# Kernel optimization log

Measured on AMD Instinct MI355X. Metric: run time of the kernel, lower is better.

## Reference

```python
import math
import jax, jax.numpy as jnp
import numpy as np

D_MODEL = 1024
L_MAX = 4096
BATCH = 2
FILTER_ORDER = 64
EMB_DIM = 3


def _make_z(L, emb_dim=EMB_DIM):
    # PositionalEmbedding: [time, real bands, imag bands] -> [1, L, emb_dim]
    t = jnp.linspace(0.0, 1.0, L)[None, :, None]
    bands = (emb_dim - 1) // 2
    t_res = jnp.linspace(0.0, L - 1.0, L)[None, :, None]
    w = 2.0 * math.pi * t_res / L
    f = jnp.linspace(1e-4, float(bands - 1), bands)[None, None]
    ph = f * w  # z = exp(-1j*ph) -> real=cos(ph), imag=-sin(ph)
    return jnp.concatenate([t, jnp.cos(ph), -jnp.sin(ph)], axis=-1).astype(jnp.float32)


def setup_inputs() -> dict:
    key = jax.random.key(0)
    ks = jax.random.split(key, 16)
    d = D_MODEL
    iw = 3 * d  # inner_width = d_model * (order + 1), order=2

    def rn(k, shape, scale):
        return (jax.random.normal(k, shape) * scale).astype(jnp.float32)

    return {
        'u': rn(ks[0], (BATCH, L_MAX, d), 1.0),
        'w_in': rn(ks[1], (iw, d), d ** -0.5),
        'b_in': rn(ks[2], (iw,), 0.01),
        'sf_w': rn(ks[3], (iw, 1, 3), 3 ** -0.5),
        'sf_b': rn(ks[4], (iw,), 0.01),
        'z': _make_z(L_MAX),
        'w0': rn(ks[5], (FILTER_ORDER, EMB_DIM), EMB_DIM ** -0.5),
        'b0': rn(ks[6], (FILTER_ORDER,), 0.01),
        'freq': jnp.ones((1, FILTER_ORDER), dtype=jnp.float32),  # Sin(w=1)
        'w1': rn(ks[7], (FILTER_ORDER, FILTER_ORDER), FILTER_ORDER ** -0.5),
        'b1': rn(ks[8], (FILTER_ORDER,), 0.01),
        'w2': rn(ks[9], (FILTER_ORDER, FILTER_ORDER), FILTER_ORDER ** -0.5),
        'b2': rn(ks[10], (FILTER_ORDER,), 0.01),
        'wf': rn(ks[11], (d, FILTER_ORDER), FILTER_ORDER ** -0.5),
        'D': rn(ks[12], (d,), 1.0),
        'w_out': rn(ks[13], (d, d), d ** -0.5),
        'b_out': rn(ks[14], (d,), 0.01),
    }


def _dwconv(x, w, b):
    # depthwise Conv1d(kernel=3, padding=2, groups=C); x: [B, C, L] -> [B, C, L+2]
    y = jax.lax.conv_general_dilated(
        x, w, window_strides=(1,), padding=[(2, 2)],
        feature_group_count=x.shape[1],
        dimension_numbers=('NCH', 'OIH', 'NCH'))
    return y + b[None, :, None]


def _fftconv(v, k, D):
    # circular conv via zero-padded FFT; torch's k_f/fft_size with norm='forward'
    # irfft cancels to the standard (norm='backward') inverse.
    L = v.shape[-1]
    n = 2 * L
    y = jnp.fft.irfft(jnp.fft.rfft(v, n=n) * jnp.fft.rfft(k, n=n), n=n)[..., :L]
    return y + v * D[:, None]


def reference(u, w_in, b_in, sf_w, sf_b, z, w0, b0, freq, w1, b1, w2, b2, wf, D, w_out, b_out):
    b, l, d = u.shape
    L = min(l, L_MAX)

    # input projection + short depthwise filter
    up = jnp.einsum('bld,ed->ble', u, w_in) + b_in  # [b, l, 3d]
    up = up.transpose(0, 2, 1)                       # [b, 3d, l]
    uc = _dwconv(up, sf_w, sf_b)[..., :L]            # [b, 3d, L]
    x0, x1, v = jnp.split(uc, 3, axis=1)             # each [b, d, L]

    # implicit filter MLP with shared Sin activation
    h = jnp.sin(freq * (z @ w0.T + b0))              # [1, L, 64]
    h = jnp.sin(freq * (h @ w1.T + b1))
    h = jnp.sin(freq * (h @ w2.T + b2))
    h = h @ wf.T                                     # [1, L, d]

    # exponential modulation (buffers: t, deltas)
    t = jnp.linspace(0.0, 1.0, L)[None, :, None]
    max_decay = math.log(0.01) / 0.3
    min_decay = math.log(0.01) / 1.5
    deltas = jnp.linspace(min_decay, max_decay, d)[None, None]
    h = h * jnp.exp(-t * jnp.abs(deltas))            # [1, L, d]
    k = h[0].T                                       # [d, L]

    # hyena recurrence (order=2 -> one gated fft conv)
    v = _fftconv(v * x1, k, D)
    y = (v * x0).transpose(0, 2, 1)                  # [b, L, d]
    return jnp.einsum('bld,ed->ble', y, w_out) + b_out
```

## Files before the change

kernel.cpp:

```cpp
#include <hip/hip_runtime.h>
#include <math.h>

#define DM   1024
#define LL   4096
#define NB   2
#define E3   3072
#define FPI  3.14159265358979323846f

typedef __bf16 bf16x8 __attribute__((ext_vector_type(8)));
typedef float  f32x4  __attribute__((ext_vector_type(4)));
typedef _Float16 f16x2 __attribute__((ext_vector_type(2)));

__device__ __forceinline__ unsigned short f2bf(float x) {
    unsigned u = __float_as_uint(x);
    u += 0x7fffu + ((u >> 16) & 1u);
    return (unsigned short)(u >> 16);
}
__device__ __forceinline__ float bf2f(ushort s) {
    return __uint_as_float(((unsigned)s) << 16);
}
__device__ __forceinline__ void gload16(void* lds, const void* g) {
    typedef const __attribute__((address_space(1))) unsigned int* gp_t;
    typedef __attribute__((address_space(3))) unsigned int* lp_t;
    __builtin_amdgcn_global_load_lds((gp_t)g, (lp_t)lds, 16, 0, 0);
}

__global__ __launch_bounds__(256) void k_cvt3(
    const float* __restrict__ a, ushort* __restrict__ oa, int n4a,
    const float* __restrict__ b, ushort* __restrict__ ob, int n4b,
    const float* __restrict__ c, ushort* __restrict__ oc, int n4c)
{
    int idx = blockIdx.x * 256 + threadIdx.x;
    int stride = gridDim.x * 256;
    int tot = n4a + n4b + n4c;
    for (int i = idx; i < tot; i += stride) {
        const float4* src; ushort* dst; int k;
        if (i < n4a)            { src = (const float4*)a; dst = oa; k = i; }
        else if (i < n4a + n4b) { src = (const float4*)b; dst = ob; k = i - n4a; }
        else                    { src = (const float4*)c; dst = oc; k = i - n4a - n4b; }
        float4 v = src[k];
        ushort4 o;
        o.x = f2bf(v.x); o.y = f2bf(v.y); o.z = f2bf(v.z); o.w = f2bf(v.w);
        *reinterpret_cast<ushort4*>(dst + 4 * k) = o;
    }
}

__global__ __launch_bounds__(512, 1) void k_gemm128n(
    const ushort* __restrict__ A, const ushort* __restrict__ B,
    const float* __restrict__ bias, ushort* __restrict__ C,
    int Ntiles, int ldc)
{
    __shared__ __align__(16) char ldsm[98304];
    const int tid  = threadIdx.x;
    const int lane = tid & 63;
    const int w    = tid >> 6;
    const int wr   = w >> 2, wc = w & 3;

    const int cpx = gridDim.x >> 3;
    int swz = (blockIdx.x & 7) * cpx + (blockIdx.x >> 3);
    const int m0 = (swz / Ntiles) << 7;
    const int n0 = (swz % Ntiles) << 8;

    const int r0 = tid >> 2;
    const int swzc = ((tid & 3) ^ ((r0 >> 1) & 3)) << 4;
    const char* Asrc = (const char*)A + ((size_t)(m0 + r0) << 11) + swzc;
    const char* Bsrc = (const char*)B + ((size_t)(n0 + r0) << 11) + swzc;
    char* Ld = ldsm + tid * 16;

    const int lm = lane & 15, lk = lane >> 4;
    const int rA = wr * 64 + lm;
    const int rB = wc * 64 + lm;
    const int aBase = rA * 64 + ((lk ^ ((rA >> 1) & 3)) << 4);
    const int bBase = 16384 + rB * 64 + ((lk ^ ((rB >> 1) & 3)) << 4);

#define STG_A(ks, nb, t1) \
    gload16(Ld + (nb) + (ks)*8192, Asrc + (t1)*128 + (ks)*64)
#define STG_B(ks, nb, t1) do { \
    gload16(Ld + (nb) + 16384 + (ks)*16384,        Bsrc + (t1)*128 + (ks)*64); \
    gload16(Ld + (nb) + 16384 + (ks)*16384 + 8192, Bsrc + (t1)*128 + (ks)*64 + 262144); } while(0)
#define LDA(buf, ks, m) (*(const bf16x8*)(ldsm + (buf) + (ks)*8192 + aBase + (m)*1024))
#define LDB(buf, ks, n) (*(const bf16x8*)(ldsm + (buf) + (ks)*16384 + bBase + (n)*1024))
#define VMCNT3() asm volatile("s_waitcnt vmcnt(3)" ::: "memory")
#define VMCNT0() asm volatile("s_waitcnt vmcnt(0)" ::: "memory")
#define BAR() __builtin_amdgcn_s_barrier()

    f32x4 acc[4][4];
#pragma unroll
    for (int i = 0; i < 4; ++i)
#pragma unroll
        for (int j = 0; j < 4; ++j)
#pragma unroll
            for (int r = 0; r < 4; ++r) acc[i][j][r] = 0.f;

    STG_A(0, 0, 0); STG_B(0, 0, 0); STG_A(1, 0, 0); STG_B(1, 0, 0);
    VMCNT3();
    BAR();

    bf16x8 af[2], bq[4];
#pragma unroll 1
    for (int t = 0; t < 15; ++t) {
        const int buf = (t & 1) * 49152;
        const int nb  = 49152 - buf;
        const int t1  = t + 1;
#pragma unroll
        for (int n = 0; n < 4; ++n) bq[n] = LDB(buf, 0, n);
        af[0] = LDA(buf, 0, 0); af[1] = LDA(buf, 0, 1);
        STG_A(0, nb, t1);
        BAR();
        __builtin_amdgcn_s_setprio(1);
#pragma unroll
        for (int m = 0; m < 2; ++m)
#pragma unroll
            for (int n = 0; n < 4; ++n)
                acc[m][n] = __builtin_amdgcn_mfma_f32_16x16x32_bf16(af[m], bq[n], acc[m][n], 0, 0, 0);
        __builtin_amdgcn_s_setprio(0);
        BAR();
        af[0] = LDA(buf, 0, 2); af[1] = LDA(buf, 0, 3);
        STG_B(0, nb, t1);
        VMCNT3();
        BAR();
        __builtin_amdgcn_s_setprio(1);
#pragma unroll
        for (int m = 0; m < 2; ++m)
#pragma unroll
            for (int n = 0; n < 4; ++n)
                acc[2 + m][n] = __builtin_amdgcn_mfma_f32_16x16x32_bf16(af[m], bq[n], acc[2 + m][n], 0, 0, 0);
        __builtin_amdgcn_s_setprio(0);
        BAR();
#pragma unroll
        for (int n = 0; n < 4; ++n) bq[n] = LDB(buf, 1, n);
        af[0] = LDA(buf, 1, 0); af[1] = LDA(buf, 1, 1);
        STG_A(1, nb, t1);
        BAR();
        __builtin_amdgcn_s_setprio(1);
#pragma unroll
        for (int m = 0; m < 2; ++m)
#pragma unroll
            for (int n = 0; n < 4; ++n)
                acc[m][n] = __builtin_amdgcn_mfma_f32_16x16x32_bf16(af[m], bq[n], acc[m][n], 0, 0, 0);
        __builtin_amdgcn_s_setprio(0);
        BAR();
        af[0] = LDA(buf, 1, 2); af[1] = LDA(buf, 1, 3);
        STG_B(1, nb, t1);
        VMCNT3();
        BAR();
        __builtin_amdgcn_s_setprio(1);
#pragma unroll
        for (int m = 0; m < 2; ++m)
#pragma unroll
            for (int n = 0; n < 4; ++n)
                acc[2 + m][n] = __builtin_amdgcn_mfma_f32_16x16x32_bf16(af[m], bq[n], acc[2 + m][n], 0, 0, 0);
        __builtin_amdgcn_s_setprio(0);
        BAR();
    }
    {
        const int buf = 49152;
#pragma unroll
        for (int n = 0; n < 4; ++n) bq[n] = LDB(buf, 0, n);
        af[0] = LDA(buf, 0, 0); af[1] = LDA(buf, 0, 1);
#pragma unroll
        for (int m = 0; m < 2; ++m)
#pragma unroll
            for (int n = 0; n < 4; ++n)
                acc[m][n] = __builtin_amdgcn_mfma_f32_16x16x32_bf16(af[m], bq[n], acc[m][n], 0, 0, 0);
        af[0] = LDA(buf, 0, 2); af[1] = LDA(buf, 0, 3);
#pragma unroll
        for (int m = 0; m < 2; ++m)
#pragma unroll
            for (int n = 0; n < 4; ++n)
                acc[2 + m][n] = __builtin_amdgcn_mfma_f32_16x16x32_bf16(af[m], bq[n], acc[2 + m][n], 0, 0, 0);
        VMCNT0();
        BAR();
#pragma unroll
        for (int n = 0; n < 4; ++n) bq[n] = LDB(buf, 1, n);
        af[0] = LDA(buf, 1, 0); af[1] = LDA(buf, 1, 1);
#pragma unroll
        for (int m = 0; m < 2; ++m)
#pragma unroll
            for (int n = 0; n < 4; ++n)
                acc[m][n] = __builtin_amdgcn_mfma_f32_16x16x32_bf16(af[m], bq[n], acc[m][n], 0, 0, 0);
        af[0] = LDA(buf, 1, 2); af[1] = LDA(buf, 1, 3);
#pragma unroll
        for (int m = 0; m < 2; ++m)
#pragma unroll
            for (int n = 0; n < 4; ++n)
                acc[2 + m][n] = __builtin_amdgcn_mfma_f32_16x16x32_bf16(af[m], bq[n], acc[2 + m][n], 0, 0, 0);
    }
    const int er = lk << 2, ec = lm;
#pragma unroll
    for (int m = 0; m < 4; ++m) {
        int row = m0 + wr * 64 + m * 16 + er;
#pragma unroll
        for (int n = 0; n < 4; ++n) {
            int col = n0 + wc * 64 + n * 16 + ec;
            ushort* cp = C + (size_t)row * ldc + col;
#pragma unroll
            for (int r = 0; r < 4; ++r)
                cp[(size_t)r * ldc] = f2bf(acc[m][n][r] + bias[row + r]);
        }
    }
#undef STG_A
#undef STG_B
#undef LDA
#undef LDB
#undef VMCNT3
#undef VMCNT0
#undef BAR
}

__global__ __launch_bounds__(256) void k_gemm_bf16(
    const ushort* __restrict__ A, const ushort* __restrict__ B,
    const float* __restrict__ bias, float* __restrict__ C, int ldc)
{
    __shared__ ushort As[128 * 32];
    __shared__ ushort Bs[128 * 32];
    const int tid  = threadIdx.x;
    const int lane = tid & 63;
    const int w    = tid >> 6;
    const int wm   = (w >> 1) << 6, wn = (w & 1) << 6;
    const int m0   = blockIdx.y << 7, n0 = blockIdx.x << 7;

    f32x4 acc[4][4];
#pragma unroll
    for (int i = 0; i < 4; ++i)
#pragma unroll
        for (int j = 0; j < 4; ++j)
#pragma unroll
            for (int r = 0; r < 4; ++r) acc[i][j][r] = 0.f;

    const char* Ab = (const char*)A + ((size_t)(m0 + (tid >> 2)) << 11) + ((tid & 3) << 4);
    const char* Bb = (const char*)B + ((size_t)(n0 + (tid >> 2)) << 11) + ((tid & 3) << 4);
    char* AsD = (char*)As + tid * 16;
    char* BsD = (char*)Bs + tid * 16;
    const char* ap = (const char*)As + ((wm + (lane & 15)) << 6) + ((lane >> 4) << 4);
    const char* bp = (const char*)Bs + ((wn + (lane & 15)) << 6) + ((lane >> 4) << 4);

    for (int k0 = 0; k0 < 1024; k0 += 32) {
        __syncthreads();
        gload16(AsD,        Ab + k0 * 2);
        gload16(AsD + 4096, Ab + 131072 + k0 * 2);
        gload16(BsD,        Bb + k0 * 2);
        gload16(BsD + 4096, Bb + 131072 + k0 * 2);
        __syncthreads();
        bf16x8 af[4], bfr[4];
#pragma unroll
        for (int i = 0; i < 4; ++i) {
            af[i]  = *(const bf16x8*)(ap + (i << 10));
            bfr[i] = *(const bf16x8*)(bp + (i << 10));
        }
#pragma unroll
        for (int i = 0; i < 4; ++i)
#pragma unroll
            for (int j = 0; j < 4; ++j)
                acc[i][j] = __builtin_amdgcn_mfma_f32_16x16x32_bf16(
                    af[i], bfr[j], acc[i][j], 0, 0, 0);
    }
    const int er = (lane >> 4) << 2;
    const int ec = lane & 15;
#pragma unroll
    for (int i = 0; i < 4; ++i) {
        int row = m0 + wm + (i << 4) + er;
#pragma unroll
        for (int j = 0; j < 4; ++j) {
            int col = n0 + wn + (j << 4) + ec;
            float bz = bias[col];
            float* cp = C + (size_t)row * ldc + col;
#pragma unroll
            for (int r = 0; r < 4; ++r)
                cp[(size_t)r * ldc] = acc[i][j][r] + bz;
        }
    }
}

__global__ __launch_bounds__(256) void k_filt_mlp(
    const float* __restrict__ z, const float* __restrict__ w0,
    const float* __restrict__ b0, const float* __restrict__ fr,
    const float* __restrict__ w1, const float* __restrict__ b1,
    const float* __restrict__ w2, const float* __restrict__ b2,
    float* __restrict__ H3)
{
    __shared__ float w1t[64 * 65];
    __shared__ float w2t[64 * 65];
    __shared__ float hb[4][64];
    const int tid = threadIdx.x;
    for (int idx = tid; idx < 4096; idx += 256) {
        int j = idx >> 6, m = idx & 63;
        w1t[m*65 + j] = w1[idx];
        w2t[m*65 + j] = w2[idx];
    }
    __syncthreads();
    const int tl = tid >> 6, j = tid & 63;
    const float frj = fr[j];
    const float b0j = b0[j], b1j = b1[j], b2j = b2[j];
    const float w00 = w0[j*3+0], w01 = w0[j*3+1], w02 = w0[j*3+2];
    const int t0 = blockIdx.x * 16;
    for (int r = 0; r < 4; ++r) {
        int t = t0 + r*4 + tl;
        float z0 = z[t*3+0], z1 = z[t*3+1], z2 = z[t*3+2];
        float h = sinf(frj * (b0j + z0*w00 + z1*w01 + z2*w02));
        hb[tl][j] = h;
        __syncthreads();
        float s = b1j;
#pragma unroll
        for (int m = 0; m < 64; ++m) s = fmaf(hb[tl][m], w1t[m*65 + j], s);
        __syncthreads();
        h = sinf(frj * s);
        hb[tl][j] = h;
        __syncthreads();
        s = b2j;
#pragma unroll
        for (int m = 0; m < 64; ++m) s = fmaf(hb[tl][m], w2t[m*65 + j], s);
        h = sinf(frj * s);
        H3[(size_t)t * 64 + j] = h;
        __syncthreads();
    }
}

__global__ __launch_bounds__(256) void k_filt_k(
    const float* __restrict__ H3, const float* __restrict__ wf,
    float* __restrict__ kf)
{
    __shared__ float Hs[64][65];
    __shared__ float Ws[64][65];
    const int tid = threadIdx.x;
    const int t0 = blockIdx.x * 64, d0 = blockIdx.y * 64;
    for (int idx = tid; idx < 4096; idx += 256) {
        int r = idx >> 6, cc = idx & 63;
        Hs[r][cc] = H3[(size_t)(t0 + r) * 64 + cc];
        Ws[r][cc] = wf[(size_t)(d0 + r) * 64 + cc];
    }
    __syncthreads();
    const int tx = tid & 15, ty = tid >> 4;
    float acc[4][4];
#pragma unroll
    for (int i = 0; i < 4; ++i)
#pragma unroll
        for (int jj = 0; jj < 4; ++jj) acc[i][jj] = 0.f;
#pragma unroll
    for (int j = 0; j < 64; ++j) {
        float wv[4], hv[4];
#pragma unroll
        for (int i = 0; i < 4; ++i) wv[i] = Ws[4*ty + i][j];
#pragma unroll
        for (int i = 0; i < 4; ++i) hv[i] = Hs[4*tx + i][j];
#pragma unroll
        for (int i = 0; i < 4; ++i)
#pragma unroll
            for (int jj = 0; jj < 4; ++jj) acc[i][jj] = fmaf(wv[i], hv[jj], acc[i][jj]);
    }
    const float mind = -3.0701134573253944f;
    const float maxd = -15.350567286626972f;
#pragma unroll
    for (int i = 0; i < 4; ++i) {
        int d = d0 + 4*ty + i;
        float delta = fabsf(mind + (maxd - mind) * ((float)d / 1023.f));
#pragma unroll
        for (int jj = 0; jj < 4; ++jj) {
            int t = t0 + 4*tx + jj;
            float tn = (float)t / 4095.f;
            kf[(size_t)d * LL + t] = acc[i][jj] * expf(-tn * delta);
        }
    }
}

__device__ __forceinline__ int pidx(int p) { return p + (p >> 4); }

__device__ __forceinline__ float2 cmul(float2 a, float2 b) {
    return make_float2(a.x*b.x - a.y*b.y, a.x*b.y + a.y*b.x);
}

__device__ void fft_lds_fwd4(float2* buf, int tid) {
    int lh = 10;
#pragma unroll
    for (int h = 2048; h >= 32; h >>= 2, lh -= 2) {
        const int hh = h >> 1;
        const float rinv = -FPI / (float)h;
        __syncthreads();
#pragma unroll
        for (int r = 0; r < 4; ++r) {
            int bf = (r << 9) + tid;
            int q  = bf & (hh - 1);
            int g  = bf >> lh;
            int j  = (g << (lh + 2)) + q;
            float2 a = buf[pidx(j)];
            float2 b = buf[pidx(j + hh)];
            float2 c = buf[pidx(j + h)];
            float2 d = buf[pidx(j + h + hh)];
            float2 t0 = make_float2(a.x + c.x, a.y + c.y);
            float2 t1 = make_float2(a.x - c.x, a.y - c.y);
            float2 t2 = make_float2(b.x + d.x, b.y + d.y);
            float2 t3 = make_float2(b.y - d.y, d.x - b.x);
            float sn, cs;
            __sincosf(rinv * (float)q, &sn, &cs);
            float c2 = cs*cs - sn*sn, s2 = 2.f*cs*sn;
            float c3 = cs*c2 - sn*s2, s3 = cs*s2 + sn*c2;
            buf[pidx(j)] = make_float2(t0.x + t2.x, t0.y + t2.y);
            float2 e1 = make_float2(t0.x - t2.x, t0.y - t2.y);
            buf[pidx(j + hh)] = make_float2(e1.x*c2 - e1.y*s2, e1.x*s2 + e1.y*c2);
            float2 e2 = make_float2(t1.x + t3.x, t1.y + t3.y);
            buf[pidx(j + h)] = make_float2(e2.x*cs - e2.y*sn, e2.x*sn + e2.y*cs);
            float2 e3 = make_float2(t1.x - t3.x, t1.y - t3.y);
            buf[pidx(j + h + hh)] = make_float2(e3.x*c3 - e3.y*s3, e3.x*s3 + e3.y*c3);
        }
    }
    __syncthreads();
}

__device__ void fft_lds_inv4(float2* buf, int tid) {
    int lh = 4;
#pragma unroll
    for (int h = 32; h <= 2048; h <<= 2, lh += 2) {
        const int hh = h >> 1;
        const float rpos = FPI / (float)h;
        __syncthreads();
#pragma unroll
        for (int r = 0; r < 4; ++r) {
            int bf = (r << 9) + tid;
            int q  = bf & (hh - 1);
            int g  = bf >> lh;
            int j  = (g << (lh + 2)) + q;
            float2 o0 = buf[pidx(j)];
            float2 o1 = buf[pidx(j + hh)];
            float2 o2 = buf[pidx(j + h)];
            float2 o3 = buf[pidx(j + h + hh)];
            float sn, cs;
            __sincosf(rpos * (float)q, &sn, &cs);
            float c2 = cs*cs - sn*sn, s2 = 2.f*cs*sn;
            float c3 = cs*c2 - sn*s2, s3 = cs*s2 + sn*c2;
            float2 p1 = make_float2(o1.x*c2 - o1.y*s2, o1.x*s2 + o1.y*c2);
            float2 p2 = make_float2(o2.x*cs - o2.y*sn, o2.x*sn + o2.y*cs);
            float2 p3 = make_float2(o3.x*c3 - o3.y*s3, o3.x*s3 + o3.y*c3);
            float2 u0 = make_float2(o0.x + p1.x, o0.y + p1.y);
            float2 u1 = make_float2(o0.x - p1.x, o0.y - p1.y);
            float2 u2 = make_float2(p2.x + p3.x, p2.y + p3.y);
            float2 u3 = make_float2(p2.x - p3.x, p2.y - p3.y);
            float2 ib = make_float2(-u3.y, u3.x);
            buf[pidx(j)]          = make_float2(u0.x + u2.x, u0.y + u2.y);
            buf[pidx(j + hh)]     = make_float2(u1.x + ib.x, u1.y + ib.y);
            buf[pidx(j + h)]      = make_float2(u0.x - u2.x, u0.y - u2.y);
            buf[pidx(j + h + hh)] = make_float2(u1.x - ib.x, u1.y - ib.y);
        }
    }
    __syncthreads();
}

__device__ __forceinline__ void fft_reg_fwd(float2* c) {
    const float W16r[8] = {1.f, 0.92387953f, 0.70710678f, 0.38268343f,
                           0.f, -0.38268343f, -0.70710678f, -0.92387953f};
    const float W16i[8] = {0.f, -0.38268343f, -0.70710678f, -0.92387953f,
                           -1.f, -0.92387953f, -0.70710678f, -0.38268343f};
#pragma unroll
    for (int k = 0; k < 8; ++k) {
        float2 a = c[k], b = c[k+8];
        float2 d = make_float2(a.x - b.x, a.y - b.y);
        c[k]   = make_float2(a.x + b.x, a.y + b.y);
        c[k+8] = cmul(d, make_float2(W16r[k], W16i[k]));
    }
    const float W8r[4] = {1.f, 0.70710678f, 0.f, -0.70710678f};
    const float W8i[4] = {0.f, -0.70710678f, -1.f, -0.70710678f};
#pragma unroll
    for (int blk = 0; blk < 16; blk += 8)
#pragma unroll
        for (int k = 0; k < 4; ++k) {
            float2 a = c[blk+k], b = c[blk+k+4];
            float2 d = make_float2(a.x - b.x, a.y - b.y);
            c[blk+k]   = make_float2(a.x + b.x, a.y + b.y);
            c[blk+k+4] = cmul(d, make_float2(W8r[k], W8i[k]));
        }
#pragma unroll
    for (int blk = 0; blk < 16; blk += 4) {
        {   float2 a = c[blk], b = c[blk+2];
            c[blk]   = make_float2(a.x + b.x, a.y + b.y);
            c[blk+2] = make_float2(a.x - b.x, a.y - b.y); }
        {   float2 a = c[blk+1], b = c[blk+3];
            float2 d = make_float2(a.x - b.x, a.y - b.y);
            c[blk+1] = make_float2(a.x + b.x, a.y + b.y);
            c[blk+3] = make_float2(d.y, -d.x); }
    }
#pragma unroll
    for (int blk = 0; blk < 16; blk += 2) {
        float2 a = c[blk], b = c[blk+1];
        c[blk]   = make_float2(a.x + b.x, a.y + b.y);
        c[blk+1] = make_float2(a.x - b.x, a.y - b.y);
    }
}

__device__ __forceinline__ void fft_reg_inv(float2* c) {
#pragma unroll
    for (int blk = 0; blk < 16; blk += 2) {
        float2 a = c[blk], b = c[blk+1];
        c[blk]   = make_float2(a.x + b.x, a.y + b.y);
        c[blk+1] = make_float2(a.x - b.x, a.y - b.y);
    }
#pragma unroll
    for (int blk = 0; blk < 16; blk += 4) {
        {   float2 a = c[blk], b = c[blk+2];
            c[blk]   = make_float2(a.x + b.x, a.y + b.y);
            c[blk+2] = make_float2(a.x - b.x, a.y - b.y); }
        {   float2 a = c[blk+1], b = c[blk+3];
            float2 bt = make_float2(-c[blk+3].y, c[blk+3].x);
            c[blk+1] = make_float2(a.x + bt.x, a.y + bt.y);
            c[blk+3] = make_float2(a.x - bt.x, a.y - bt.y); }
    }
    const float W8r[4] = {1.f, 0.70710678f, 0.f, -0.70710678f};
    const float W8i[4] = {0.f, 0.70710678f, 1.f, 0.70710678f};
#pragma unroll
    for (int blk = 0; blk < 16; blk += 8)
#pragma unroll
        for (int k = 0; k < 4; ++k) {
            float2 a = c[blk+k], b = c[blk+k+4];
            float2 bt = cmul(b, make_float2(W8r[k], W8i[k]));
            c[blk+k]   = make_float2(a.x + bt.x, a.y + bt.y);
            c[blk+k+4] = make_float2(a.x - bt.x, a.y - bt.y);
        }
    const float W16r[8] = {1.f, 0.92387953f, 0.70710678f, 0.38268343f,
                           0.f, -0.38268343f, -0.70710678f, -0.92387953f};
    const float W16i[8] = {0.f, 0.38268343f, 0.70710678f, 0.92387953f,
                           1.f, 0.92387953f, 0.70710678f, 0.38268343f};
#pragma unroll
    for (int k = 0; k < 8; ++k) {
        float2 a = c[k], b = c[k+8];
        float2 bt = cmul(b, make_float2(W16r[k], W16i[k]));
        c[k]   = make_float2(a.x + bt.x, a.y + bt.y);
        c[k+8] = make_float2(a.x - bt.x, a.y - bt.y);
    }
}

__global__ __launch_bounds__(512) void k_kfft(
    const float* __restrict__ kf, f16x2* __restrict__ Kf)
{
    __shared__ float2 buf[8704];
    const int d = blockIdx.x, tid = threadIdx.x;
    const float* krow = kf + (size_t)d * LL;
    const float rinv0 = -FPI / 4096.f;
    for (int i = tid; i < 1024; i += 512) {
        float4 k4 = reinterpret_cast<const float4*>(krow)[i];
        int p = 4 * i;
        float kv[4] = {k4.x, k4.y, k4.z, k4.w};
#pragma unroll
        for (int q = 0; q < 4; ++q) {
            float sn, cs;
            __sincosf(rinv0 * (float)(p + q), &sn, &cs);
            buf[pidx(p + q)]        = make_float2(kv[q], 0.f);
            buf[pidx(p + q + 4096)] = make_float2(kv[q] * cs, kv[q] * sn);
        }
    }
    fft_lds_fwd4(buf, tid);
    float2 c[16];
    const int p0 = tid * 16;
#pragma unroll
    for (int j = 0; j < 16; ++j) c[j] = buf[pidx(p0 + j)];
    fft_reg_fwd(c);
    f16x2* outp = Kf + (size_t)d * 8192 + p0;
#pragma unroll
    for (int j = 0; j < 16; ++j) {
        f16x2 o;
        o[0] = (_Float16)(c[j].x * (1.f/8192.f));
        o[1] = (_Float16)(c[j].y * (1.f/8192.f));
        outp[j] = o;
    }
}

__device__ __forceinline__ void conv4(const ushort* __restrict__ row, int p,
    float w0, float w1, float w2, float bias, float* out)
{
    float xm2, xm1;
    if (p >= 2) {
        unsigned prev = *reinterpret_cast<const unsigned*>(row + p - 2);
        xm2 = bf2f((ushort)(prev & 0xffffu));
        xm1 = bf2f((ushort)(prev >> 16));
    } else { xm2 = 0.f; xm1 = 0.f; }
    uint2 cur = *reinterpret_cast<const uint2*>(row + p);
    float x0 = bf2f((ushort)(cur.x & 0xffffu));
    float x1 = bf2f((ushort)(cur.x >> 16));
    float x2 = bf2f((ushort)(cur.y & 0xffffu));
    float x3 = bf2f((ushort)(cur.y >> 16));
    out[0] = fmaf(w2, x0, fmaf(w1, xm1, fmaf(w0, xm2, bias)));
    out[1] = fmaf(w2, x1, fmaf(w1, x0,  fmaf(w0, xm1, bias)));
    out[2] = fmaf(w2, x2, fmaf(w1, x1,  fmaf(w0, x0,  bias)));
    out[3] = fmaf(w2, x3, fmaf(w1, x2,  fmaf(w0, x1,  bias)));
}

__global__ __launch_bounds__(512) void k_fftconv(
    const ushort* __restrict__ up2, const f16x2* __restrict__ Kf,
    const float* __restrict__ sfw, const float* __restrict__ sfb,
    const float* __restrict__ Dp, ushort* __restrict__ yg)
{
    __shared__ float2 buf[8704];
    const int d = blockIdx.x, tid = threadIdx.x;
    const ushort* vrow0  = up2 + (size_t)(2048 + d) * 8192;
    const ushort* vrow1  = vrow0 + 4096;
    const ushort* x1row0 = up2 + (size_t)(1024 + d) * 8192;
    const ushort* x1row1 = x1row0 + 4096;
    const ushort* x0row0 = up2 + (size_t)d * 8192;
    const ushort* x0row1 = x0row0 + 4096;
    const float wv0 = sfw[(2048+d)*3+0], wv1 = sfw[(2048+d)*3+1],
                wv2 = sfw[(2048+d)*3+2], bv = sfb[2048+d];
    const float wx0 = sfw[(1024+d)*3+0], wx1 = sfw[(1024+d)*3+1],
                wx2 = sfw[(1024+d)*3+2], bx = sfb[1024+d];
    const float g0 = sfw[d*3+0], g1 = sfw[d*3+1], g2 = sfw[d*3+2], bg = sfb[d];
    const float rinv0 = -FPI / 4096.f;

    float vs0[8], vs1[8];
#pragma unroll
    for (int ii = 0; ii < 2; ++ii) {
        int p = 4 * tid + ii * 2048;
        float cv0[4], cv1[4], cx0[4], cx1[4];
        conv4(vrow0,  p, wv0, wv1, wv2, bv, cv0);
        conv4(vrow1,  p, wv0, wv1, wv2, bv, cv1);
        conv4(x1row0, p, wx0, wx1, wx2, bx, cx0);
        conv4(x1row1, p, wx0, wx1, wx2, bx, cx1);
#pragma unroll
        for (int q = 0; q < 4; ++q) {
            float z0 = cv0[q] * cx0[q];
            float z1 = cv1[q] * cx1[q];
            vs0[ii*4 + q] = z0;
            vs1[ii*4 + q] = z1;
            float sn, cs;
            __sincosf(rinv0 * (float)(p + q), &sn, &cs);
            float2 z = make_float2(z0, z1);
            buf[pidx(p + q)]        = z;
            buf[pidx(p + q + 4096)] = cmul(z, make_float2(cs, sn));
        }
    }
    fft_lds_fwd4(buf, tid);
    float2 c[16];
    const int p0 = tid * 16;
#pragma unroll
    for (int j = 0; j < 16; ++j) c[j] = buf[pidx(p0 + j)];
    fft_reg_fwd(c);
    const f16x2* kfr = Kf + (size_t)d * 8192 + p0;
#pragma unroll
    for (int j = 0; j < 16; ++j) {
        f16x2 kv = kfr[j];
        c[j] = cmul(c[j], make_float2((float)kv[0], (float)kv[1]));
    }
    fft_reg_inv(c);
#pragma unroll
    for (int j = 0; j < 16; ++j) buf[pidx(p0 + j)] = c[j];
    fft_lds_inv4(buf, tid);
    const float Dd = Dp[d];
    ushort* orow0 = yg + (size_t)d * LL;
    ushort* orow1 = yg + ((size_t)DM + d) * LL;
    const float rinv4 = FPI / 4096.f;
#pragma unroll
    for (int ii = 0; ii < 2; ++ii) {
        int p = 4 * tid + ii * 2048;
        float cg0[4], cg1[4];
        conv4(x0row0, p, g0, g1, g2, bg, cg0);
        conv4(x0row1, p, g0, g1, g2, bg, cg1);
        ushort s0[4], s1[4];
#pragma unroll
        for (int q = 0; q < 4; ++q) {
            float sn, cs;
            __sincosf(rinv4 * (float)(p + q), &sn, &cs);
            float2 a  = buf[pidx(p + q)];
            float2 bb = buf[pidx(p + q + 4096)];
            float2 bt = cmul(bb, make_float2(cs, sn));
            s0[q] = f2bf((a.x + bt.x + Dd * vs0[ii*4 + q]) * cg0[q]);
            s1[q] = f2bf((a.y + bt.y + Dd * vs1[ii*4 + q]) * cg1[q]);
        }
        *reinterpret_cast<ushort4*>(orow0 + p) = make_ushort4(s0[0], s0[1], s0[2], s0[3]);
        *reinterpret_cast<ushort4*>(orow1 + p) = make_ushort4(s1[0], s1[1], s1[2], s1[3]);
    }
}

__global__ __launch_bounds__(256) void k_tr(
    const ushort* __restrict__ yg, ushort* __restrict__ Ag)
{
    __shared__ ushort S[64][72];
    const int b  = blockIdx.z;
    const int d0 = blockIdx.y * 64;
    const int t0 = blockIdx.x * 64;
    const int tid = threadIdx.x;
#pragma unroll
    for (int p = 0; p < 2; ++p) {
        int idx = p * 256 + tid;
        int dr = idx >> 3, c8 = (idx & 7) << 3;
        uint4 v = *reinterpret_cast<const uint4*>(
            yg + ((size_t)b * DM + d0 + dr) * LL + t0 + c8);
        *reinterpret_cast<uint4*>(&S[dr][c8]) = v;
    }
    __syncthreads();
#pragma unroll
    for (int p = 0; p < 2; ++p) {
        int idx = p * 256 + tid;
        int tr = idx >> 3, dq = (idx & 7) << 3;
        ushort tmp[8] __attribute__((aligned(16)));
#pragma unroll
        for (int q = 0; q < 8; ++q) tmp[q] = S[dq + q][tr];
        *reinterpret_cast<uint4*>(Ag + ((size_t)b * LL + t0 + tr) * DM + d0 + dq) =
            *reinterpret_cast<uint4*>(tmp);
    }
}

extern "C" void kernel_launch(void* const* d_in, const int* in_sizes, int n_in,
                              void* d_out, int out_size, void* d_ws, size_t ws_size,
                              hipStream_t stream)
{
    if (n_in < 17) return;
    const float* u    = (const float*)d_in[0];
    const float* w_in = (const float*)d_in[1];
    const float* b_in = (const float*)d_in[2];
    const float* sf_w = (const float*)d_in[3];
    const float* sf_b = (const float*)d_in[4];
    const float* z    = (const float*)d_in[5];
    const float* w0   = (const float*)d_in[6];
    const float* b0   = (const float*)d_in[7];
    const float* freq = (const float*)d_in[8];
    const float* w1   = (const float*)d_in[9];
    const float* b1   = (const float*)d_in[10];
    const float* w2   = (const float*)d_in[11];
    const float* b2   = (const float*)d_in[12];
    const float* wf   = (const float*)d_in[13];
    const float* Dp   = (const float*)d_in[14];
    const float* wout = (const float*)d_in[15];
    const float* bout = (const float*)d_in[16];
    float* out = (float*)d_out;
    float* ws  = (float*)d_ws;

    ushort* up2   = (ushort*)ws;
    float*  kfbuf = ws + 16777216;
    ushort* yg    = (ushort*)(ws + 16777216);
    float*  H3    = ws + 20971520;
    ushort* Ag    = (ushort*)(ws + 20971520);
    ushort* ub    = (ushort*)(ws + 25165824);
    ushort* wb    = (ushort*)(ws + 33554432);
    f16x2*  Kf    = (f16x2*)(ws + 33554432);
    ushort* woutb = (ushort*)(ws + 41943040);
    const size_t NEED = (size_t)(41943040 + 524288) * 4;
    if (ws_size < NEED) return;

    hipLaunchKernelGGL(k_cvt3,     dim3(2048), dim3(256), 0, stream,
                       u, ub, 2097152, w_in, wb, 786432, wout, woutb, 262144);
    hipLaunchKernelGGL(k_gemm128n, dim3((E3/128) * (8192/256)), dim3(512), 0, stream,
                       wb, ub, b_in, up2, 8192/256, 8192);
    hipLaunchKernelGGL(k_filt_mlp, dim3(LL/16), dim3(256), 0, stream,
                       z, w0, b0, freq, w1, b1, w2, b2, H3);
    hipLaunchKernelGGL(k_filt_k,   dim3(LL/64, DM/64), dim3(256), 0, stream,
                       H3, wf, kfbuf);
    hipLaunchKernelGGL(k_kfft,     dim3(DM), dim3(512), 0, stream,
                       kfbuf, Kf);
    hipLaunchKernelGGL(k_fftconv,  dim3(DM), dim3(512), 0, stream,
                       up2, Kf, sf_w, sf_b, Dp, yg);
    hipLaunchKernelGGL(k_tr,       dim3(LL/64, DM/64, NB), dim3(256), 0, stream,
                       yg, Ag);
    hipLaunchKernelGGL(k_gemm_bf16, dim3(DM/128, 8192/128), dim3(256), 0, stream,
                       Ag, woutb, bout, out, DM);
}
```

Baseline: 223.8 us.

## Fuse filter FFT into fftconv kernel and remap GEMM tiles per XCD

The separate k_kfft kernel is removed. Each fftconv block now computes its own filter spectrum in LDS and keeps it in registers, which drops the fp16 spectrum write and read and one kernel launch. To limit register pressure, the saved v*x1 values are recomputed from up2 in the epilogue instead of being held across the FFTs. The input-projection GEMM's block-to-tile mapping is changed so each XCD owns a contiguous range of N tiles. The costs are more VGPR use from the 16 held complex values and extra reloads for the recompute.

Result: no change. 224.3 us (+0.2%).

```diff
diff --git a/kernel.cpp b/kernel.cpp
--- a/kernel.cpp
+++ b/kernel.cpp
@@ -9,7 +9,6 @@
 
 typedef __bf16 bf16x8 __attribute__((ext_vector_type(8)));
 typedef float  f32x4  __attribute__((ext_vector_type(4)));
-typedef _Float16 f16x2 __attribute__((ext_vector_type(2)));
 
 __device__ __forceinline__ unsigned short f2bf(float x) {
     unsigned u = __float_as_uint(x);
@@ -56,10 +55,11 @@
     const int w    = tid >> 6;
     const int wr   = w >> 2, wc = w & 3;
 
-    const int cpx = gridDim.x >> 3;
-    int swz = (blockIdx.x & 7) * cpx + (blockIdx.x >> 3);
-    const int m0 = (swz / Ntiles) << 7;
-    const int n0 = (swz % Ntiles) << 8;
+    const int nch = Ntiles >> 3;
+    const int xcd = blockIdx.x & 7;
+    const int loc = blockIdx.x >> 3;
+    const int n0 = ((xcd * nch) + (loc % nch)) << 8;
+    const int m0 = (loc / nch) << 7;
 
     const int r0 = tid >> 2;
     const int swzc = ((tid & 3) ^ ((r0 >> 1) & 3)) << 4;
@@ -526,41 +526,6 @@
     }
 }
 
-__global__ __launch_bounds__(512) void k_kfft(
-    const float* __restrict__ kf, f16x2* __restrict__ Kf)
-{
-    __shared__ float2 buf[8704];
-    const int d = blockIdx.x, tid = threadIdx.x;
-    const float* krow = kf + (size_t)d * LL;
-    const float rinv0 = -FPI / 4096.f;
-    for (int i = tid; i < 1024; i += 512) {
-        float4 k4 = reinterpret_cast<const float4*>(krow)[i];
-        int p = 4 * i;
-        float kv[4] = {k4.x, k4.y, k4.z, k4.w};
-#pragma unroll
-        for (int q = 0; q < 4; ++q) {
-            float sn, cs;
-            __sincosf(rinv0 * (float)(p + q), &sn, &cs);
-            buf[pidx(p + q)]        = make_float2(kv[q], 0.f);
-            buf[pidx(p + q + 4096)] = make_float2(kv[q] * cs, kv[q] * sn);
-        }
-    }
-    fft_lds_fwd4(buf, tid);
-    float2 c[16];
-    const int p0 = tid * 16;
-#pragma unroll
-    for (int j = 0; j < 16; ++j) c[j] = buf[pidx(p0 + j)];
-    fft_reg_fwd(c);
-    f16x2* outp = Kf + (size_t)d * 8192 + p0;
-#pragma unroll
-    for (int j = 0; j < 16; ++j) {
-        f16x2 o;
-        o[0] = (_Float16)(c[j].x * (1.f/8192.f));
-        o[1] = (_Float16)(c[j].y * (1.f/8192.f));
-        outp[j] = o;
-    }
-}
-
 __device__ __forceinline__ void conv4(const ushort* __restrict__ row, int p,
     float w0, float w1, float w2, float bias, float* out)
 {
@@ -582,12 +547,40 @@
 }
 
 __global__ __launch_bounds__(512) void k_fftconv(
-    const ushort* __restrict__ up2, const f16x2* __restrict__ Kf,
+    const float* __restrict__ kfrow_all, const ushort* __restrict__ up2,
     const float* __restrict__ sfw, const float* __restrict__ sfb,
     const float* __restrict__ Dp, ushort* __restrict__ yg)
 {
     __shared__ float2 buf[8704];
     const int d = blockIdx.x, tid = threadIdx.x;
+    const float rinv0 = -FPI / 4096.f;
+    const int p0 = tid * 16;
+
+    {
+        const float* krow = kfrow_all + (size_t)d * LL;
+#pragma unroll
+        for (int ii = 0; ii < 2; ++ii) {
+            int i = tid + ii * 512;
+            float4 k4 = reinterpret_cast<const float4*>(krow)[i];
+            int p = 4 * i;
+            float kv[4] = {k4.x * (1.f/8192.f), k4.y * (1.f/8192.f),
+                           k4.z * (1.f/8192.f), k4.w * (1.f/8192.f)};
+#pragma unroll
+            for (int q = 0; q < 4; ++q) {
+                float sn, cs;
+                __sincosf(rinv0 * (float)(p + q), &sn, &cs);
+                buf[pidx(p + q)]        = make_float2(kv[q], 0.f);
+                buf[pidx(p + q + 4096)] = make_float2(kv[q] * cs, kv[q] * sn);
+            }
+        }
+    }
+    fft_lds_fwd4(buf, tid);
+    float2 ks[16];
+#pragma unroll
+    for (int j = 0; j < 16; ++j) ks[j] = buf[pidx(p0 + j)];
+    fft_reg_fwd(ks);
+    __syncthreads();
+
     const ushort* vrow0  = up2 + (size_t)(2048 + d) * 8192;
     const ushort* vrow1  = vrow0 + 4096;
     const ushort* x1row0 = up2 + (size_t)(1024 + d) * 8192;
@@ -599,9 +592,7 @@
     const float wx0 = sfw[(1024+d)*3+0], wx1 = sfw[(1024+d)*3+1],
                 wx2 = sfw[(1024+d)*3+2], bx = sfb[1024+d];
     const float g0 = sfw[d*3+0], g1 = sfw[d*3+1], g2 = sfw[d*3+2], bg = sfb[d];
-    const float rinv0 = -FPI / 4096.f;
-
-    float vs0[8], vs1[8];
+
 #pragma unroll
     for (int ii = 0; ii < 2; ++ii) {
         int p = 4 * tid + ii * 2048;
@@ -614,8 +605,6 @@
         for (int q = 0; q < 4; ++q) {
             float z0 = cv0[q] * cx0[q];
             float z1 = cv1[q] * cx1[q];
-            vs0[ii*4 + q] = z0;
-            vs1[ii*4 + q] = z1;
             float sn, cs;
             __sincosf(rinv0 * (float)(p + q), &sn, &cs);
             float2 z = make_float2(z0, z1);
@@ -625,16 +614,11 @@
     }
     fft_lds_fwd4(buf, tid);
     float2 c[16];
-    const int p0 = tid * 16;
 #pragma unroll
     for (int j = 0; j < 16; ++j) c[j] = buf[pidx(p0 + j)];
     fft_reg_fwd(c);
-    const f16x2* kfr = Kf + (size_t)d * 8192 + p0;
-#pragma unroll
-    for (int j = 0; j < 16; ++j) {
-        f16x2 kv = kfr[j];
-        c[j] = cmul(c[j], make_float2((float)kv[0], (float)kv[1]));
-    }
+#pragma unroll
+    for (int j = 0; j < 16; ++j) c[j] = cmul(c[j], ks[j]);
     fft_reg_inv(c);
 #pragma unroll
     for (int j = 0; j < 16; ++j) buf[pidx(p0 + j)] = c[j];
@@ -646,9 +630,13 @@
 #pragma unroll
     for (int ii = 0; ii < 2; ++ii) {
         int p = 4 * tid + ii * 2048;
-        float cg0[4], cg1[4];
+        float cg0[4], cg1[4], cv0[4], cv1[4], cx0[4], cx1[4];
         conv4(x0row0, p, g0, g1, g2, bg, cg0);
         conv4(x0row1, p, g0, g1, g2, bg, cg1);
+        conv4(vrow0,  p, wv0, wv1, wv2, bv, cv0);
+        conv4(vrow1,  p, wv0, wv1, wv2, bv, cv1);
+        conv4(x1row0, p, wx0, wx1, wx2, bx, cx0);
+        conv4(x1row1, p, wx0, wx1, wx2, bx, cx1);
         ushort s0[4], s1[4];
 #pragma unroll
         for (int q = 0; q < 4; ++q) {
@@ -657,8 +645,8 @@
             float2 a  = buf[pidx(p + q)];
             float2 bb = buf[pidx(p + q + 4096)];
             float2 bt = cmul(bb, make_float2(cs, sn));
-            s0[q] = f2bf((a.x + bt.x + Dd * vs0[ii*4 + q]) * cg0[q]);
-            s1[q] = f2bf((a.y + bt.y + Dd * vs1[ii*4 + q]) * cg1[q]);
+            s0[q] = f2bf((a.x + bt.x + Dd * cv0[q] * cx0[q]) * cg0[q]);
+            s1[q] = f2bf((a.y + bt.y + Dd * cv1[q] * cx1[q]) * cg1[q]);
         }
         *reinterpret_cast<ushort4*>(orow0 + p) = make_ushort4(s0[0], s0[1], s0[2], s0[3]);
         *reinterpret_cast<ushort4*>(orow1 + p) = make_ushort4(s1[0], s1[1], s1[2], s1[3]);
@@ -721,12 +709,11 @@
 
     ushort* up2   = (ushort*)ws;
     float*  kfbuf = ws + 16777216;
-    ushort* yg    = (ushort*)(ws + 16777216);
     float*  H3    = ws + 20971520;
     ushort* Ag    = (ushort*)(ws + 20971520);
     ushort* ub    = (ushort*)(ws + 25165824);
     ushort* wb    = (ushort*)(ws + 33554432);
-    f16x2*  Kf    = (f16x2*)(ws + 33554432);
+    ushort* yg    = (ushort*)(ws + 33554432);
     ushort* woutb = (ushort*)(ws + 41943040);
     const size_t NEED = (size_t)(41943040 + 524288) * 4;
     if (ws_size < NEED) return;
@@ -739,10 +726,8 @@
                        z, w0, b0, freq, w1, b1, w2, b2, H3);
     hipLaunchKernelGGL(k_filt_k,   dim3(LL/64, DM/64), dim3(256), 0, stream,
                        H3, wf, kfbuf);
-    hipLaunchKernelGGL(k_kfft,     dim3(DM), dim3(512), 0, stream,
-                       kfbuf, Kf);
     hipLaunchKernelGGL(k_fftconv,  dim3(DM), dim3(512), 0, stream,
-                       up2, Kf, sf_w, sf_b, Dp, yg);
+                       kfbuf, up2, sf_w, sf_b, Dp, yg);
     hipLaunchKernelGGL(k_tr,       dim3(LL/64, DM/64, NB), dim3(256), 0, stream,
                        yg, Ag);
     hipLaunchKernelGGL(k_gemm_bf16, dim3(DM/128, 8192/128), dim3(256), 0, stream,
```
